# Kernel tuning notes

Measured on AMD Instinct MI355X. Metric: run time of the kernel, lower is better.

Reference implementation:

```python
import jax, jax.numpy as jnp
import numpy as np

D_IN = 1024
D_OUT = 1024
NUM_HEADS = 16
HEAD_DIM = D_OUT // NUM_HEADS
CONTEXT_LEN = 2048


def setup_inputs() -> dict:
    key = jax.random.key(0)
    ks = jax.random.split(key, 7)
    scale = 0.02
    x = jax.random.normal(ks[0], (2, 2048, D_IN), dtype=jnp.float32)
    Wq = jax.random.normal(ks[1], (D_IN, D_OUT), dtype=jnp.float32) * scale
    bq = jnp.zeros((D_OUT,), dtype=jnp.float32)
    Wk = jax.random.normal(ks[2], (D_IN, D_OUT), dtype=jnp.float32) * scale
    bk = jnp.zeros((D_OUT,), dtype=jnp.float32)
    Wv = jax.random.normal(ks[3], (D_IN, D_OUT), dtype=jnp.float32) * scale
    bv = jnp.zeros((D_OUT,), dtype=jnp.float32)
    return {"x": x, "Wq": Wq, "bq": bq, "Wk": Wk, "bk": bk, "Wv": Wv, "bv": bv}


def reference(x, Wq, bq, Wk, bk, Wv, bv):
    B, S, _ = x.shape
    # QKV projections with bias
    q = x @ Wq + bq  # [B,S,D_OUT]
    k = x @ Wk + bk
    v = x @ Wv + bv
    # split heads -> [B,H,S,Dh]
    def heads(t):
        return t.reshape(B, S, NUM_HEADS, HEAD_DIM).transpose(0, 2, 1, 3)
    q, k, v = heads(q), heads(k), heads(v)
    # raw scores, then additive causal mask (-1e9 on strictly upper triangle),
    # then scale by 1/sqrt(head_dim) AFTER adding mask (matches original code)
    scores = jnp.einsum("bhqd,bhkd->bhqk", q, k)
    causal = jnp.tril(jnp.ones((S, S), dtype=bool))
    add_mask = jnp.where(causal, 0.0, -1e9).astype(scores.dtype)
    scores = scores + add_mask
    weights = jax.nn.softmax(scores / jnp.sqrt(jnp.asarray(HEAD_DIM, scores.dtype)), axis=-1)
    ctx = jnp.einsum("bhqk,bhkd->bhqd", weights, v)  # [B,H,S,Dh]
    return ctx.transpose(0, 2, 1, 3).reshape(B, S, D_OUT)
```

## Files before the change

### kernel.cpp

```cpp
#include <hip/hip_runtime.h>
#include <hip/hip_bf16.h>
#include <stdint.h>

#define D_IN 1024
#define NH 16
#define DH 64
#define SEQ 2048
#define BATCH 2

typedef unsigned short u16;
typedef __attribute__((ext_vector_type(8))) short short8;
typedef __attribute__((ext_vector_type(4))) float f32x4;

#define CSCALE 0.1803368801f

__device__ __forceinline__ u16 f2bf(float f) {
    union { float f; uint32_t u; } v; v.f = f;
    uint32_t r = v.u + 0x7FFF + ((v.u >> 16) & 1);
    return (u16)(r >> 16);
}

__device__ __forceinline__ float bf2f(u16 u) {
    union { uint32_t u; float f; } v; v.u = (uint32_t)u << 16;
    return v.f;
}

__device__ __forceinline__ uint32_t pktrunc(float a, float b) {
    union { float f; uint32_t u; } x, y;
    x.f = a; y.f = b;
    return __builtin_amdgcn_perm(y.u, x.u, 0x07060302u);
}

__device__ __forceinline__ void async16(const u16* g, u16* l) {
    __builtin_amdgcn_global_load_lds(
        (const __attribute__((address_space(1))) void*)g,
        (__attribute__((address_space(3))) void*)l, 16, 0, 0);
}

__global__ __launch_bounds__(256) void prep_kernel(
    const float* __restrict__ x, const float* __restrict__ Wq,
    const float* __restrict__ Wk, const float* __restrict__ Wv,
    u16* __restrict__ xb, u16* __restrict__ WT)
{
    __shared__ float tile[64][65];
    if (blockIdx.x < 4096) {
        int i = (blockIdx.x * 256 + threadIdx.x) * 4;
        float4 v = *(const float4*)(x + i);
        union { u16 u[4]; uint2 d; } o;
        o.u[0] = f2bf(v.x); o.u[1] = f2bf(v.y); o.u[2] = f2bf(v.z); o.u[3] = f2bf(v.w);
        *(uint2*)(xb + i) = o.d;
        return;
    }
    int idx = blockIdx.x - 4096;
    int mat = idx >> 8, rem = idx & 255;
    int k0 = (rem & 15) * 64, n0 = (rem >> 4) * 64;
    const float* W = (mat == 0) ? Wq : (mat == 1 ? Wk : Wv);
    int c = threadIdx.x & 63, rb = threadIdx.x >> 6;
    #pragma unroll
    for (int p = 0; p < 16; ++p) {
        int r = p * 4 + rb;
        tile[r][c] = W[(size_t)(k0 + r) * 1024 + n0 + c];
    }
    __syncthreads();
    #pragma unroll
    for (int p = 0; p < 16; ++p) {
        int r = p * 4 + rb;
        WT[((size_t)mat * 1024 + n0 + r) * 1024 + k0 + c] = f2bf(tile[c][r]);
    }
}

__global__ __launch_bounds__(256) void qkv_gemm_kernel(
    const u16* __restrict__ xb, const u16* __restrict__ WT,
    const float* __restrict__ bq, const float* __restrict__ bk,
    const float* __restrict__ bv,
    u16* __restrict__ Qb, u16* __restrict__ Kb, u16* __restrict__ Vt)
{
    __shared__ u16 smem[4 * 64 * 72];
    u16* As = smem;
    u16* Bs = smem + 128 * 64;
    const int tid  = threadIdx.x;
    const int wave = tid >> 6, lane = tid & 63;
    const int quad = lane >> 4, l15 = lane & 15;
    const int m0 = blockIdx.y * 128;
    const int n0 = blockIdx.x * 128;

    f32x4 acc[4][4];
    #pragma unroll
    for (int i = 0; i < 4; ++i)
        #pragma unroll
        for (int j = 0; j < 4; ++j)
            acc[i][j] = (f32x4){0.f, 0.f, 0.f, 0.f};

    const int wm = wave & 1, wn = wave >> 1;
    const int srow8 = tid >> 3;
    const int sslot = tid & 7;
    const int fsig  = l15 & 7;

    for (int k0 = 0; k0 < 1024; k0 += 64) {
        #pragma unroll
        for (int rnd = 0; rnd < 4; ++rnd) {
            int row = rnd * 32 + srow8;
            int g = sslot ^ (row & 7);
            async16(xb + (size_t)(m0 + row) * 1024 + k0 + g * 8, As + rnd * 2048 + tid * 8);
            async16(WT + (size_t)(n0 + row) * 1024 + k0 + g * 8, Bs + rnd * 2048 + tid * 8);
        }
        __syncthreads();
        #pragma unroll
        for (int kk = 0; kk < 2; ++kk) {
            short8 af[4], bfr[4];
            #pragma unroll
            for (int f = 0; f < 4; ++f) {
                int slot = ((kk << 2) + quad) ^ fsig;
                af[f]  = *(const short8*)(As + (wm * 64 + f * 16 + l15) * 64 + slot * 8);
                bfr[f] = *(const short8*)(Bs + (wn * 64 + f * 16 + l15) * 64 + slot * 8);
            }
            #pragma unroll
            for (int i = 0; i < 4; ++i)
                #pragma unroll
                for (int j = 0; j < 4; ++j)
                    acc[i][j] = __builtin_amdgcn_mfma_f32_16x16x32_bf16(af[i], bfr[j], acc[i][j], 0, 0, 0);
        }
        __syncthreads();
    }

    const int mat = n0 >> 10;
    const int ncb = (n0 & 1023) + wn * 64;
    const int hh = ncb >> 6;
    const int bb = m0 >> 11, sb = m0 & 2047;

    if (mat < 2) {
        const float* bias = (mat == 0) ? bq : bk;
        u16* dst = (mat == 0) ? Qb : Kb;
        const float sc = (mat == 0) ? CSCALE : 1.0f;
        #pragma unroll
        for (int i = 0; i < 4; ++i) {
            int ss = sb + wm * 64 + i * 16 + quad * 4;
            #pragma unroll
            for (int j = 0; j < 4; ++j) {
                int dh = j * 16 + l15;
                float bval = bias[ncb + dh];
                size_t base = (((size_t)bb * NH + hh) * SEQ + ss) * DH + dh;
                #pragma unroll
                for (int r = 0; r < 4; ++r)
                    dst[base + (size_t)r * DH] = f2bf((acc[i][j][r] + bval) * sc);
            }
        }
    } else {
        u16* vt = smem + wave * (64 * 72);
        #pragma unroll
        for (int i = 0; i < 4; ++i)
            #pragma unroll
            for (int j = 0; j < 4; ++j) {
                float bval = bv[ncb + j * 16 + l15];
                union { u16 u[4]; uint2 d; } o;
                #pragma unroll
                for (int r = 0; r < 4; ++r)
                    o.u[r] = f2bf(acc[i][j][r] + bval);
                *(uint2*)(vt + (j * 16 + l15) * 72 + i * 16 + quad * 4) = o.d;
            }
        const int s0w = sb + wm * 64;
        u16* vdst = Vt + ((size_t)(bb * NH + hh) * DH) * SEQ;
        #pragma unroll
        for (int it = 0; it < 8; ++it) {
            int dh = it * 8 + (lane >> 3);
            short8 v = *(const short8*)(vt + dh * 72 + (lane & 7) * 8);
            *(short8*)(vdst + (size_t)dh * SEQ + s0w + (lane & 7) * 8) = v;
        }
    }
}

__device__ __forceinline__ void stage64(const u16* g0, size_t gstride, u16* lds,
                                        int wave, int lane)
{
    #pragma unroll
    for (int rnd = 0; rnd < 2; ++rnd) {
        int row = rnd * 32 + wave * 8 + (lane >> 3);
        int sig = ((row >> 3) & 1) * 4 + (row & 3);
        int c = (lane & 7) ^ sig;
        async16(g0 + (size_t)row * gstride + c * 8, lds + row * 64 + (lane & 7) * 8);
    }
}

__global__ __launch_bounds__(256) void flash_mfma_kernel(
    const u16* __restrict__ Qb, const u16* __restrict__ Kb,
    const u16* __restrict__ Vt, float* __restrict__ out,
    u16* __restrict__ Opart, float* __restrict__ Lpart)
{
    static const int JQT[24] = {7,15,15,14,14, 6,13,13,12,12, 5,11,11,10,10,
                                4, 9, 9, 8, 8, 3, 2, 1, 0};
    static const int JHF[24] = {-1,0,1,0,1, -1,0,1,0,1, -1,0,1,0,1,
                                -1,0,1,0,1, -1,-1,-1,-1};

    __shared__ u16 Ks[2][64 * 64];
    __shared__ u16 Vs[2][64 * 64];

    const int tid  = threadIdx.x;
    const int wave = tid >> 6, lane = tid & 63;
    const int quad = lane >> 4, l15 = lane & 15;
    const int bhx = blockIdx.x;
    const int b = bhx >> 4, h = bhx & 15;
    const int job = blockIdx.y;
    const int qt = JQT[job], hf = JHF[job];
    const int t0 = (hf == 1) ? qt + 1 : 0;
    const int t1 = (hf == 0) ? qt + 1 : 2 * qt + 2;
    const int q0 = qt * 128;
    const int wq0 = wave * 32;
    const size_t bh = (size_t)bhx;
    const u16* Qp = Qb + bh * SEQ * DH;
    const u16* Kp = Kb + bh * SEQ * DH;
    const u16* Vp = Vt + bh * DH * SEQ;

    short8 qf[2][2];
    #pragma unroll
    for (int qa = 0; qa < 2; ++qa) {
        const u16* qrp = Qp + (size_t)(q0 + wq0 + qa * 16 + l15) * DH;
        qf[qa][0] = *(const short8*)(qrp + quad * 8);
        qf[qa][1] = *(const short8*)(qrp + 32 + quad * 8);
    }

    const short8 ones = (short8){0x3F80, 0x3F80, 0x3F80, 0x3F80,
                                 0x3F80, 0x3F80, 0x3F80, 0x3F80};

    f32x4 O[2][4], L[2];
    #pragma unroll
    for (int pa = 0; pa < 2; ++pa) {
        #pragma unroll
        for (int f = 0; f < 4; ++f) O[pa][f] = (f32x4){0.f, 0.f, 0.f, 0.f};
        L[pa] = (f32x4){0.f, 0.f, 0.f, 0.f};
    }

    const int wqmax = q0 + wq0 + 31;
    const int krbase = (l15 >> 2) * 8 + (l15 & 3);
    const int ksig   = ((l15 >> 2) & 1) * 4 + (l15 & 3);
    const int vsig   = ((l15 >> 3) & 1) * 4 + (l15 & 3);

    stage64(Kp + (size_t)t0 * 64 * DH, DH, Ks[t0 & 1], wave, lane);
    stage64(Vp + t0 * 64, SEQ, Vs[t0 & 1], wave, lane);
    __syncthreads();

    for (int t = t0; t < t1; ++t) {
        const int cur = t & 1;
        if (t + 1 < t1) {
            int k1 = (t + 1) * 64;
            stage64(Kp + (size_t)k1 * DH, DH, Ks[cur ^ 1], wave, lane);
            stage64(Vp + k1, SEQ, Vs[cur ^ 1], wave, lane);
        }
        const int k0 = t * 64;
        if (k0 <= wqmax) {
            f32x4 sf[4][2];
            #pragma unroll
            for (int fj = 0; fj < 4; ++fj) {
                int krow = (fj >> 1) * 32 + krbase + (fj & 1) * 4;
                const u16* kp = &Ks[cur][krow * 64];
                short8 k0f = *(const short8*)(kp + (quad ^ ksig) * 8);
                short8 k1f = *(const short8*)(kp + ((4 + quad) ^ ksig) * 8);
                #pragma unroll
                for (int qa = 0; qa < 2; ++qa) {
                    f32x4 s = (f32x4){0.f, 0.f, 0.f, 0.f};
                    s = __builtin_amdgcn_mfma_f32_16x16x32_bf16(k0f, qf[qa][0], s, 0, 0, 0);
                    s = __builtin_amdgcn_mfma_f32_16x16x32_bf16(k1f, qf[qa][1], s, 0, 0, 0);
                    sf[fj][qa] = s;
                }
            }
            const bool diag = (k0 + 63 > q0 + wq0);
            short8 pA[2][2];
            #pragma unroll
            for (int qa = 0; qa < 2; ++qa) {
                #pragma unroll
                for (int fj = 0; fj < 4; ++fj)
                    #pragma unroll
                    for (int r = 0; r < 4; ++r) {
                        float p = __builtin_amdgcn_exp2f(sf[fj][qa][r]);
                        if (diag) {
                            int key = k0 + (fj >> 1) * 32 + quad * 8 + (fj & 1) * 4 + r;
                            int qg  = q0 + wq0 + qa * 16 + l15;
                            p = (key <= qg) ? p : 0.f;
                        }
                        sf[fj][qa][r] = p;
                    }
                union { uint32_t d[4]; short8 v; } a0, a1;
                a0.d[0] = pktrunc(sf[0][qa][0], sf[0][qa][1]);
                a0.d[1] = pktrunc(sf[0][qa][2], sf[0][qa][3]);
                a0.d[2] = pktrunc(sf[1][qa][0], sf[1][qa][1]);
                a0.d[3] = pktrunc(sf[1][qa][2], sf[1][qa][3]);
                a1.d[0] = pktrunc(sf[2][qa][0], sf[2][qa][1]);
                a1.d[1] = pktrunc(sf[2][qa][2], sf[2][qa][3]);
                a1.d[2] = pktrunc(sf[3][qa][0], sf[3][qa][1]);
                a1.d[3] = pktrunc(sf[3][qa][2], sf[3][qa][3]);
                pA[qa][0] = a0.v;
                pA[qa][1] = a1.v;
                L[qa] = __builtin_amdgcn_mfma_f32_16x16x32_bf16(pA[qa][0], ones, L[qa], 0, 0, 0);
                L[qa] = __builtin_amdgcn_mfma_f32_16x16x32_bf16(pA[qa][1], ones, L[qa], 0, 0, 0);
            }
            #pragma unroll
            for (int fo = 0; fo < 4; ++fo) {
                const u16* vrow = &Vs[cur][(fo * 16 + l15) * 64];
                short8 vb0 = *(const short8*)(vrow + (quad ^ vsig) * 8);
                short8 vb1 = *(const short8*)(vrow + ((4 + quad) ^ vsig) * 8);
                #pragma unroll
                for (int pa = 0; pa < 2; ++pa) {
                    O[pa][fo] = __builtin_amdgcn_mfma_f32_16x16x32_bf16(pA[pa][0], vb0, O[pa][fo], 0, 0, 0);
                    O[pa][fo] = __builtin_amdgcn_mfma_f32_16x16x32_bf16(pA[pa][1], vb1, O[pa][fo], 0, 0, 0);
                }
            }
        }
        __syncthreads();
    }

    if (hf < 0) {
        #pragma unroll
        for (int pa = 0; pa < 2; ++pa)
            #pragma unroll
            for (int fo = 0; fo < 4; ++fo)
                #pragma unroll
                for (int r = 0; r < 4; ++r) {
                    int s = q0 + wq0 + pa * 16 + quad * 4 + r;
                    out[((size_t)b * SEQ + s) * 1024 + h * DH + fo * 16 + l15] =
                        O[pa][fo][r] / L[pa][r];
                }
    } else {
        const int pi = (qt - 8) * 2 + hf;
        u16* op = Opart + (((size_t)pi * 32 + bhx) * 128) * 64;
        float* lp = Lpart + ((size_t)pi * 32 + bhx) * 128;
        #pragma unroll
        for (int pa = 0; pa < 2; ++pa) {
            #pragma unroll
            for (int fo = 0; fo < 4; ++fo)
                #pragma unroll
                for (int r = 0; r < 4; ++r) {
                    int ql = wq0 + pa * 16 + quad * 4 + r;
                    op[(size_t)ql * 64 + fo * 16 + l15] = f2bf(O[pa][fo][r]);
                }
            if (l15 == 0) {
                #pragma unroll
                for (int r = 0; r < 4; ++r)
                    lp[wq0 + pa * 16 + quad * 4 + r] = L[pa][r];
            }
        }
    }
}

__global__ __launch_bounds__(256) void combine_kernel(
    const u16* __restrict__ Opart, const float* __restrict__ Lpart,
    float* __restrict__ out)
{
    int blk = blockIdx.x;
    int qt = 8 + (blk >> 5);
    int bh = blk & 31;
    int b = bh >> 4, h = bh & 15;
    int pi0 = (qt - 8) * 2, pi1 = pi0 + 1;
    int tid = threadIdx.x;
    int q = tid >> 1, seg = (tid & 1) * 32;
    const u16* o0 = Opart + (((size_t)pi0 * 32 + bh) * 128 + q) * 64 + seg;
    const u16* o1 = Opart + (((size_t)pi1 * 32 + bh) * 128 + q) * 64 + seg;
    float inv = 1.0f / (Lpart[((size_t)pi0 * 32 + bh) * 128 + q] +
                        Lpart[((size_t)pi1 * 32 + bh) * 128 + q]);
    float* op = out + ((size_t)b * SEQ + qt * 128 + q) * 1024 + h * DH + seg;
    #pragma unroll
    for (int d = 0; d < 32; d += 4) {
        union { uint2 d2; u16 u[4]; } a, c;
        a.d2 = *(const uint2*)(o0 + d);
        c.d2 = *(const uint2*)(o1 + d);
        float4 v;
        v.x = (bf2f(a.u[0]) + bf2f(c.u[0])) * inv;
        v.y = (bf2f(a.u[1]) + bf2f(c.u[1])) * inv;
        v.z = (bf2f(a.u[2]) + bf2f(c.u[2])) * inv;
        v.w = (bf2f(a.u[3]) + bf2f(c.u[3])) * inv;
        *(float4*)(op + d) = v;
    }
}

extern "C" void kernel_launch(void* const* d_in, const int* in_sizes, int n_in,
                              void* d_out, int out_size, void* d_ws, size_t ws_size,
                              hipStream_t stream) {
    const float* x  = (const float*)d_in[0];
    const float* Wq = (const float*)d_in[1];
    const float* bq = (const float*)d_in[2];
    const float* Wk = (const float*)d_in[3];
    const float* bk = (const float*)d_in[4];
    const float* Wv = (const float*)d_in[5];
    const float* bv = (const float*)d_in[6];
    float* out = (float*)d_out;

    const size_t NX = (size_t)BATCH * SEQ * D_IN;
    const size_t NW = (size_t)3 * D_IN * 1024;
    const size_t NP = (size_t)BATCH * NH * SEQ * DH;
    u16* xb = (u16*)d_ws;
    u16* WT = xb + NX;
    u16* Qb = WT + NW;
    u16* Kb = Qb + NP;
    u16* Vt = Kb + NP;
    u16* Opart = xb;
    float* Lpart = (float*)(xb + NX);

    prep_kernel<<<4096 + 768, 256, 0, stream>>>(x, Wq, Wk, Wv, xb, WT);
    qkv_gemm_kernel<<<dim3(24, 32), 256, 0, stream>>>(xb, WT, bq, bk, bv, Qb, Kb, Vt);
    flash_mfma_kernel<<<dim3(32, 24), 256, 0, stream>>>(Qb, Kb, Vt, out, Opart, Lpart);
    combine_kernel<<<256, 256, 0, stream>>>(Opart, Lpart, out);
}
```

Baseline: 162.3 us.

## Split KV range across two wave groups in one block, combine in LDS

The flash attention kernel now runs 512 threads per block. Two groups of four waves each cover half of the key range for the same 128-query tile and merge their partial outputs and row sums through shared memory. This replaces the earlier job table of split blocks plus a separate combine kernel that round-tripped bf16 partials through global memory, removing one launch and that traffic. In exchange the grid shrinks to 512 blocks, LDS use per block rises, and tiles with little work still hold a full 512-thread block.

```diff
diff --git a/kernel.cpp b/kernel.cpp
--- a/kernel.cpp
+++ b/kernel.cpp
@@ -18,11 +18,6 @@
     union { float f; uint32_t u; } v; v.f = f;
     uint32_t r = v.u + 0x7FFF + ((v.u >> 16) & 1);
     return (u16)(r >> 16);
-}
-
-__device__ __forceinline__ float bf2f(u16 u) {
-    union { uint32_t u; float f; } v; v.u = (uint32_t)u << 16;
-    return v.f;
 }
 
 __device__ __forceinline__ uint32_t pktrunc(float a, float b) {
@@ -170,46 +165,40 @@
 }
 
 __device__ __forceinline__ void stage64(const u16* g0, size_t gstride, u16* lds,
-                                        int wave, int lane)
+                                        int w4, int lane)
 {
     #pragma unroll
     for (int rnd = 0; rnd < 2; ++rnd) {
-        int row = rnd * 32 + wave * 8 + (lane >> 3);
+        int row = rnd * 32 + w4 * 8 + (lane >> 3);
         int sig = ((row >> 3) & 1) * 4 + (row & 3);
         int c = (lane & 7) ^ sig;
         async16(g0 + (size_t)row * gstride + c * 8, lds + row * 64 + (lane & 7) * 8);
     }
 }
 
-__global__ __launch_bounds__(256) void flash_mfma_kernel(
+__global__ __launch_bounds__(512) void flash_mfma_kernel(
     const u16* __restrict__ Qb, const u16* __restrict__ Kb,
-    const u16* __restrict__ Vt, float* __restrict__ out,
-    u16* __restrict__ Opart, float* __restrict__ Lpart)
+    const u16* __restrict__ Vt, float* __restrict__ out)
 {
-    static const int JQT[24] = {7,15,15,14,14, 6,13,13,12,12, 5,11,11,10,10,
-                                4, 9, 9, 8, 8, 3, 2, 1, 0};
-    static const int JHF[24] = {-1,0,1,0,1, -1,0,1,0,1, -1,0,1,0,1,
-                                -1,0,1,0,1, -1,-1,-1,-1};
-
-    __shared__ u16 Ks[2][64 * 64];
-    __shared__ u16 Vs[2][64 * 64];
+    __shared__ u16 smem[8 * 4096];
 
     const int tid  = threadIdx.x;
     const int wave = tid >> 6, lane = tid & 63;
+    const int grp  = wave >> 2, w4 = wave & 3;
     const int quad = lane >> 4, l15 = lane & 15;
     const int bhx = blockIdx.x;
     const int b = bhx >> 4, h = bhx & 15;
-    const int job = blockIdx.y;
-    const int qt = JQT[job], hf = JHF[job];
-    const int t0 = (hf == 1) ? qt + 1 : 0;
-    const int t1 = (hf == 0) ? qt + 1 : 2 * qt + 2;
+    const int qt = (blockIdx.y < 8) ? (15 - (int)blockIdx.y) : ((int)blockIdx.y - 8);
     const int q0 = qt * 128;
-    const int wq0 = wave * 32;
+    const int wq0 = w4 * 32;
     const size_t bh = (size_t)bhx;
     const u16* Qp = Qb + bh * SEQ * DH;
     const u16* Kp = Kb + bh * SEQ * DH;
     const u16* Vp = Vt + bh * DH * SEQ;
 
+    u16* Kg[2] = { smem + (grp * 2 + 0) * 4096, smem + (grp * 2 + 1) * 4096 };
+    u16* Vg[2] = { smem + 16384 + (grp * 2 + 0) * 4096, smem + 16384 + (grp * 2 + 1) * 4096 };
+
     short8 qf[2][2];
     #pragma unroll
     for (int qa = 0; qa < 2; ++qa) {
@@ -234,16 +223,20 @@
     const int ksig   = ((l15 >> 2) & 1) * 4 + (l15 & 3);
     const int vsig   = ((l15 >> 3) & 1) * 4 + (l15 & 3);
 
-    stage64(Kp + (size_t)t0 * 64 * DH, DH, Ks[t0 & 1], wave, lane);
-    stage64(Vp + t0 * 64, SEQ, Vs[t0 & 1], wave, lane);
+    const int niter = qt + 1;
+    const int tbase = grp ? (qt + 1) : 0;
+
+    stage64(Kp + (size_t)tbase * 64 * DH, DH, Kg[0], w4, lane);
+    stage64(Vp + tbase * 64, SEQ, Vg[0], w4, lane);
     __syncthreads();
 
-    for (int t = t0; t < t1; ++t) {
-        const int cur = t & 1;
-        if (t + 1 < t1) {
+    for (int i = 0; i < niter; ++i) {
+        const int t = tbase + i;
+        const int cur = i & 1;
+        if (i + 1 < niter) {
             int k1 = (t + 1) * 64;
-            stage64(Kp + (size_t)k1 * DH, DH, Ks[cur ^ 1], wave, lane);
-            stage64(Vp + k1, SEQ, Vs[cur ^ 1], wave, lane);
+            stage64(Kp + (size_t)k1 * DH, DH, Kg[cur ^ 1], w4, lane);
+            stage64(Vp + k1, SEQ, Vg[cur ^ 1], w4, lane);
         }
         const int k0 = t * 64;
         if (k0 <= wqmax) {
@@ -251,7 +244,7 @@
             #pragma unroll
             for (int fj = 0; fj < 4; ++fj) {
                 int krow = (fj >> 1) * 32 + krbase + (fj & 1) * 4;
-                const u16* kp = &Ks[cur][krow * 64];
+                const u16* kp = Kg[cur] + krow * 64;
                 short8 k0f = *(const short8*)(kp + (quad ^ ksig) * 8);
                 short8 k1f = *(const short8*)(kp + ((4 + quad) ^ ksig) * 8);
                 #pragma unroll
@@ -294,7 +287,7 @@
             }
             #pragma unroll
             for (int fo = 0; fo < 4; ++fo) {
-                const u16* vrow = &Vs[cur][(fo * 16 + l15) * 64];
+                const u16* vrow = Vg[cur] + (fo * 16 + l15) * 64;
                 short8 vb0 = *(const short8*)(vrow + (quad ^ vsig) * 8);
                 short8 vb1 = *(const short8*)(vrow + ((4 + quad) ^ vsig) * 8);
                 #pragma unroll
@@ -307,66 +300,40 @@
         __syncthreads();
     }
 
-    if (hf < 0) {
-        #pragma unroll
-        for (int pa = 0; pa < 2; ++pa)
+    float* Osh = (float*)smem;
+    float* Lsh = Osh + 128 * 66;
+    if (grp == 0) {
+        #pragma unroll
+        for (int pa = 0; pa < 2; ++pa) {
             #pragma unroll
             for (int fo = 0; fo < 4; ++fo)
                 #pragma unroll
+                for (int r = 0; r < 4; ++r)
+                    Osh[(wq0 + pa * 16 + quad * 4 + r) * 66 + fo * 16 + l15] = O[pa][fo][r];
+            if (l15 == 0) {
+                #pragma unroll
+                for (int r = 0; r < 4; ++r)
+                    Lsh[wq0 + pa * 16 + quad * 4 + r] = L[pa][r];
+            }
+        }
+    }
+    __syncthreads();
+    if (grp == 1) {
+        #pragma unroll
+        for (int pa = 0; pa < 2; ++pa) {
+            float lt[4];
+            #pragma unroll
+            for (int r = 0; r < 4; ++r)
+                lt[r] = L[pa][r] + Lsh[wq0 + pa * 16 + quad * 4 + r];
+            #pragma unroll
+            for (int fo = 0; fo < 4; ++fo)
+                #pragma unroll
                 for (int r = 0; r < 4; ++r) {
-                    int s = q0 + wq0 + pa * 16 + quad * 4 + r;
-                    out[((size_t)b * SEQ + s) * 1024 + h * DH + fo * 16 + l15] =
-                        O[pa][fo][r] / L[pa][r];
+                    int q = wq0 + pa * 16 + quad * 4 + r;
+                    float o = O[pa][fo][r] + Osh[q * 66 + fo * 16 + l15];
+                    out[((size_t)b * SEQ + q0 + q) * 1024 + h * DH + fo * 16 + l15] = o / lt[r];
                 }
-    } else {
-        const int pi = (qt - 8) * 2 + hf;
-        u16* op = Opart + (((size_t)pi * 32 + bhx) * 128) * 64;
-        float* lp = Lpart + ((size_t)pi * 32 + bhx) * 128;
-        #pragma unroll
-        for (int pa = 0; pa < 2; ++pa) {
-            #pragma unroll
-            for (int fo = 0; fo < 4; ++fo)
-                #pragma unroll
-                for (int r = 0; r < 4; ++r) {
-                    int ql = wq0 + pa * 16 + quad * 4 + r;
-                    op[(size_t)ql * 64 + fo * 16 + l15] = f2bf(O[pa][fo][r]);
-                }
-            if (l15 == 0) {
-                #pragma unroll
-                for (int r = 0; r < 4; ++r)
-                    lp[wq0 + pa * 16 + quad * 4 + r] = L[pa][r];
-            }
-        }
-    }
-}
-
-__global__ __launch_bounds__(256) void combine_kernel(
-    const u16* __restrict__ Opart, const float* __restrict__ Lpart,
-    float* __restrict__ out)
-{
-    int blk = blockIdx.x;
-    int qt = 8 + (blk >> 5);
-    int bh = blk & 31;
-    int b = bh >> 4, h = bh & 15;
-    int pi0 = (qt - 8) * 2, pi1 = pi0 + 1;
-    int tid = threadIdx.x;
-    int q = tid >> 1, seg = (tid & 1) * 32;
-    const u16* o0 = Opart + (((size_t)pi0 * 32 + bh) * 128 + q) * 64 + seg;
-    const u16* o1 = Opart + (((size_t)pi1 * 32 + bh) * 128 + q) * 64 + seg;
-    float inv = 1.0f / (Lpart[((size_t)pi0 * 32 + bh) * 128 + q] +
-                        Lpart[((size_t)pi1 * 32 + bh) * 128 + q]);
-    float* op = out + ((size_t)b * SEQ + qt * 128 + q) * 1024 + h * DH + seg;
-    #pragma unroll
-    for (int d = 0; d < 32; d += 4) {
-        union { uint2 d2; u16 u[4]; } a, c;
-        a.d2 = *(const uint2*)(o0 + d);
-        c.d2 = *(const uint2*)(o1 + d);
-        float4 v;
-        v.x = (bf2f(a.u[0]) + bf2f(c.u[0])) * inv;
-        v.y = (bf2f(a.u[1]) + bf2f(c.u[1])) * inv;
-        v.z = (bf2f(a.u[2]) + bf2f(c.u[2])) * inv;
-        v.w = (bf2f(a.u[3]) + bf2f(c.u[3])) * inv;
-        *(float4*)(op + d) = v;
+        }
     }
 }
 
@@ -390,11 +357,8 @@
     u16* Qb = WT + NW;
     u16* Kb = Qb + NP;
     u16* Vt = Kb + NP;
-    u16* Opart = xb;
-    float* Lpart = (float*)(xb + NX);
 
     prep_kernel<<<4096 + 768, 256, 0, stream>>>(x, Wq, Wk, Wv, xb, WT);
     qkv_gemm_kernel<<<dim3(24, 32), 256, 0, stream>>>(xb, WT, bq, bk, bv, Qb, Kb, Vt);
-    flash_mfma_kernel<<<dim3(32, 24), 256, 0, stream>>>(Qb, Kb, Vt, out, Opart, Lpart);
-    combine_kernel<<<256, 256, 0, stream>>>(Opart, Lpart, out);
-}
+    flash_mfma_kernel<<<dim3(32, 16), 512, 0, stream>>>(Qb, Kb, Vt, out);
+}
```

New measurement: 171.3 us. 1.06x slower.
